# Kernel tuning notes

Hardware: AMD Instinct MI355X
Metric: run time of the kernel (lower is better)

Reference implementation:

```python
import jax, jax.numpy as jnp
import numpy as np

DIM = 192
N_HEADS = 8
HEAD_DIM = DIM // N_HEADS
SCALE = 1.0 / np.sqrt(HEAD_DIM).astype(np.float32)
H_GRID, W_GRID = 32, 64
KH, KW = 7, 11


def build_local_mask():
    # Equivalent to the torch double-loop construction: token (h2,w2) may attend
    # to (h,w) iff |h2-h| <= KH//2 and |w2-w| <= KW//2 (odd kernels).
    hh = jnp.arange(H_GRID)
    ww = jnp.arange(W_GRID)
    dh_ok = jnp.abs(hh[:, None] - hh[None, :]) <= KH // 2  # [H, H]
    dw_ok = jnp.abs(ww[:, None] - ww[None, :]) <= KW // 2  # [W, W]
    allowed = dh_ok[:, None, :, None] & dw_ok[None, :, None, :]  # [H, W, H, W]
    allowed = allowed.reshape(H_GRID * W_GRID, H_GRID * W_GRID)
    return jnp.where(allowed, 0.0, -jnp.inf).astype(jnp.float32)  # [N, N]


def setup_inputs() -> dict:
    key = jax.random.key(0)
    ks = jax.random.split(key, 5)
    B, N = 4, H_GRID * W_GRID
    w_std = 1.0 / np.sqrt(DIM)
    x = jax.random.normal(ks[0], (B, N, DIM), dtype=jnp.float32)
    qkv_w = jax.random.normal(ks[1], (3 * DIM, DIM), dtype=jnp.float32) * w_std
    qkv_b = jax.random.normal(ks[2], (3 * DIM,), dtype=jnp.float32) * 0.02
    proj_w = jax.random.normal(ks[3], (DIM, DIM), dtype=jnp.float32) * w_std
    proj_b = jax.random.normal(ks[4], (DIM,), dtype=jnp.float32) * 0.02
    mask = build_local_mask()
    return {"x": x, "qkv_w": qkv_w, "qkv_b": qkv_b,
            "proj_w": proj_w, "proj_b": proj_b, "mask": mask}


def reference(x, qkv_w, qkv_b, proj_w, proj_b, mask):
    B, N, _ = x.shape
    qkv = x @ qkv_w.T + qkv_b                              # [B, N, 3*DIM]
    qkv = qkv.reshape(B, N, 3, N_HEADS, HEAD_DIM)
    qkv = jnp.transpose(qkv, (2, 0, 3, 1, 4))              # [3, B, h, N, d]
    q, k, v = qkv[0] * SCALE, qkv[1], qkv[2]
    attn = jnp.einsum('bhnd,bhmd->bhnm', q, k) + mask      # [B, h, N, N]
    attn = jax.nn.softmax(attn, axis=-1)                   # == log_softmax().exp()
    out = jnp.einsum('bhnm,bhmd->bhnd', attn, v)           # [B, h, N, d]
    out = jnp.transpose(out, (0, 2, 1, 3)).reshape(B, N, DIM)
    return out @ proj_w.T + proj_b
```

## Files before the change

### kernel.cpp

```cpp
#include <hip/hip_runtime.h>
#include <math.h>

#define H_GRID 32
#define W_GRID 64
#define NTOK   2048
#define NHEADS 8
#define HD     24
#define DIMC   192
#define BATCH  4

static constexpr float SCALE = 0.20412414523193154f;

typedef unsigned short ushort;
typedef unsigned int   uint;
typedef __attribute__((ext_vector_type(8))) _Float16 f16x8;
typedef __attribute__((ext_vector_type(4))) float    f32x4;

static __device__ __forceinline__ float4 ld4(const float* p) { return *(const float4*)p; }

static __device__ __forceinline__ ushort f2h(float f) {
    _Float16 h = (_Float16)f;
    union { _Float16 h; ushort u; } c; c.h = h; return c.u;
}
static __device__ __forceinline__ float h2f(ushort u) {
    union { ushort u; _Float16 h; } c; c.u = u; return (float)c.h;
}

__global__ __launch_bounds__(256) void cast_h(const float* __restrict__ x,
                                              const float* __restrict__ wq,
                                              const float* __restrict__ wp,
                                              ushort* __restrict__ xh,
                                              ushort* __restrict__ wqh,
                                              ushort* __restrict__ wph,
                                              ushort* __restrict__ Qh,
                                              ushort* __restrict__ Kh) {
    const int i = blockIdx.x * 256 + threadIdx.x;
    if (i >= 430080) {
        const int ti = i - 430080;
        ushort* dst = (ti >> 16) ? Kh : Qh;
        const int row = ti & 65535;
        const uint4 z = {0u, 0u, 0u, 0u};
        *(uint4*)&dst[(size_t)row * 32 + 24] = z;
        return;
    }
    const float* src; ushort* dh; int off;
    if (i < 393216)      { src = x;  dh = xh;  off = i; }
    else if (i < 420864) { src = wq; dh = wqh; off = i - 393216; }
    else                 { src = wp; dh = wph; off = i - 420864; }
    float4 v = ld4(src + (size_t)off * 4);
    *(ushort4*)(dh + (size_t)off * 4) =
        make_ushort4(f2h(v.x), f2h(v.y), f2h(v.z), f2h(v.w));
}

__global__ __launch_bounds__(256, 4) void gemm_qkv(const ushort* __restrict__ Ah,
                                                   const ushort* __restrict__ Wh,
                                                   const float* __restrict__ bias,
                                                   ushort* __restrict__ Qh,
                                                   ushort* __restrict__ Kh,
                                                   ushort* __restrict__ VTh) {
    __shared__ ushort Ws[64 * 200];

    const int t    = threadIdx.x;
    const int wave = t >> 6, lane = t & 63;
    const int m0   = blockIdx.x * 64 + wave * 16;
    const int j0   = blockIdx.y * 64;
    const int n16  = lane & 15;
    const int kq   = lane >> 4;

    for (int i = t; i < 1536; i += 256) {
        const int r = i / 24, c = i - (i / 24) * 24;
        *(uint4*)&Ws[r * 200 + c * 8] = *(const uint4*)&Wh[(size_t)(j0 + r) * 192 + c * 8];
    }

    const ushort* ap = Ah + (size_t)(m0 + n16) * 192 + kq * 8;

    f16x8 af[6];
#pragma unroll
    for (int ks = 0; ks < 6; ks++) af[ks] = *(const f16x8*)(ap + ks * 32);

    f32x4 acc[4] = {f32x4{0,0,0,0}, f32x4{0,0,0,0}, f32x4{0,0,0,0}, f32x4{0,0,0,0}};

    __syncthreads();

#pragma unroll
    for (int ks = 0; ks < 6; ks++) {
#pragma unroll
        for (int nt = 0; nt < 4; nt++) {
            const f16x8 bf = *(const f16x8*)&Ws[(nt * 16 + n16) * 200 + kq * 8 + ks * 32];
            acc[nt] = __builtin_amdgcn_mfma_f32_16x16x32_f16(af[ks], bf, acc[nt], 0, 0, 0);
        }
    }

    const int band  = blockIdx.y / 3;
    const int mrow0 = m0 + kq * 4;
    const int b_    = mrow0 >> 11;
    const int tok0  = mrow0 & 2047;

    if (band == 2) {
#pragma unroll
        for (int nt = 0; nt < 4; nt++) {
            const int col = j0 + nt * 16 + n16;
            const int lc  = col - 384;
            const int h_  = lc / 24;
            const int d_  = lc - h_ * 24;
            const float bv = bias[col];
            ushort vv[4];
#pragma unroll
            for (int r = 0; r < 4; r++) vv[r] = f2h(acc[nt][r] + bv);
            const size_t addr = ((size_t)(b_ * 8 + h_) * 32 + d_) * 2080 + 8 + tok0;
            *(ushort4*)&VTh[addr] = make_ushort4(vv[0], vv[1], vv[2], vv[3]);
        }
    } else {
        const float sc_ = band ? 1.0f : SCALE;
        __syncthreads();
#pragma unroll
        for (int nt = 0; nt < 4; nt++) {
            const int col = j0 + nt * 16 + n16;
            const float bv = bias[col];
#pragma unroll
            for (int r = 0; r < 4; r++) {
                Ws[(wave * 16 + kq * 4 + r) * 68 + nt * 16 + n16] =
                    f2h((acc[nt][r] + bv) * sc_);
            }
        }
        __syncthreads();
        ushort* dst = band ? Kh : Qh;
        const int lc0 = j0 - band * 192;
#pragma unroll
        for (int it = 0; it < 4; it++) {
            const int item = t + 256 * it;
            const int tokl = item >> 4;
            const int cg   = item & 15;
            const ushort4 v = *(const ushort4*)&Ws[tokl * 68 + cg * 4];
            const int lc = lc0 + cg * 4;
            const int h_ = lc / 24;
            const int d0 = lc - h_ * 24;
            const int m  = blockIdx.x * 64 + tokl;
            const size_t addr = ((size_t)((m >> 11) * 8 + h_) * 2048 + (m & 2047)) * 32 + d0;
            *(ushort4*)&dst[addr] = v;
        }
    }
}

__global__ __launch_bounds__(256, 4) void attn_mfma(const ushort* __restrict__ Qh,
                                                    const ushort* __restrict__ Kh,
                                                    const ushort* __restrict__ VTh,
                                                    ushort* __restrict__ aws) {
    const int id    = blockIdx.x;
    const int head  = id & 7;
    const int qtile = (id >> 3) & 63;
    const int b     = id >> 9;
    const int qh0   = (qtile >> 3) * 4;
    const int qw0   = (qtile & 7) * 8;
    const int kw0a  = qw0 - 8;

    const int t = threadIdx.x;
    const int w = t >> 6, lane = t & 63;
    const int n16 = lane & 15, quad = lane >> 4;
    const int bh = b * 8 + head;

    __shared__ ushort P[32 * 328];
    __shared__ ushort Os[32 * 28];
    __shared__ float  mxbuf[64], sumbuf[64];

    const ushort* Qb = Qh + (size_t)bh * 65536;
    const ushort* Kb = Kh + (size_t)bh * 65536;

    const int mt = w >> 1, nth = w & 1;
    const int mrow = 16 * mt + n16;
    const int tq_a = ((qh0 + (mrow >> 3)) << 6) + qw0 + (mrow & 7);
    const f16x8 qf = *(const f16x8*)&Qb[(size_t)tq_a * 32 + quad * 8];

    float sv[10][4];
    float mx4[4] = {-3e38f, -3e38f, -3e38f, -3e38f};
#pragma unroll
    for (int half = 0; half < 2; half++) {
        f16x8 kf[5];
        int khvv[5], kwvv[5];
#pragma unroll
        for (int jj = 0; jj < 5; jj++) {
            const int j = half * 5 + jj;
            const int slot = (nth * 10 + j) * 16 + n16;
            const int rr = slot >> 5, cc = slot & 31;
            khvv[jj] = qh0 - 3 + rr;
            kwvv[jj] = kw0a + cc;
            const int tok = (min(max(khvv[jj], 0), 31) << 6) + min(max(kwvv[jj], 0), 63);
            kf[jj] = *(const f16x8*)&Kb[(size_t)tok * 32 + quad * 8];
        }
#pragma unroll
        for (int jj = 0; jj < 5; jj++) {
            const int j = half * 5 + jj;
            f32x4 a = f32x4{0, 0, 0, 0};
            a = __builtin_amdgcn_mfma_f32_16x16x32_f16(qf, kf[jj], a, 0, 0, 0);
            const int khv = khvv[jj], kwv = kwvv[jj];
            const bool kok = (khv >= 0) && (khv < 32) && (kwv >= 0) && (kwv < 64);
#pragma unroll
            for (int r = 0; r < 4; r++) {
                const int m   = 16 * mt + quad * 4 + r;
                const int qhv = qh0 + (m >> 3);
                const int qwv = qw0 + (m & 7);
                const bool valid = kok && (abs(khv - qhv) <= 3) && (abs(kwv - qwv) <= 5);
                const float s = valid ? a[r] : -3e38f;
                sv[j][r] = s;
                mx4[r] = fmaxf(mx4[r], s);
            }
        }
    }
#pragma unroll
    for (int d = 1; d < 16; d <<= 1)
#pragma unroll
        for (int r = 0; r < 4; r++) mx4[r] = fmaxf(mx4[r], __shfl_xor(mx4[r], d));
    if (n16 == 0) {
#pragma unroll
        for (int r = 0; r < 4; r++) mxbuf[w * 16 + quad * 4 + r] = mx4[r];
    }
    __syncthreads();
#pragma unroll
    for (int r = 0; r < 4; r++) mx4[r] = fmaxf(mx4[r], mxbuf[(w ^ 1) * 16 + quad * 4 + r]);

    float sum4[4] = {0.f, 0.f, 0.f, 0.f};
#pragma unroll
    for (int j = 0; j < 10; j++) {
        const int slot = (nth * 10 + j) * 16 + n16;
#pragma unroll
        for (int r = 0; r < 4; r++) {
            const float p = __expf(sv[j][r] - mx4[r]);
            const ushort ph = f2h(p);
            sum4[r] += h2f(ph);
            P[(16 * mt + quad * 4 + r) * 328 + slot] = ph;
        }
    }
#pragma unroll
    for (int d = 1; d < 16; d <<= 1)
#pragma unroll
        for (int r = 0; r < 4; r++) sum4[r] += __shfl_xor(sum4[r], d);
    if (n16 == 0) {
#pragma unroll
        for (int r = 0; r < 4; r++) sumbuf[w * 16 + quad * 4 + r] = sum4[r];
    }
    __syncthreads();

    const int mtP = w >> 1, ntP = w & 1;
    const int dcol = 16 * ntP + n16;
    const ushort* VTb = VTh + (size_t)bh * 66560;
    f32x4 acc = f32x4{0, 0, 0, 0};
#pragma unroll
    for (int half = 0; half < 2; half++) {
        f16x8 vf[5], pa[5];
#pragma unroll
        for (int kk = 0; kk < 5; kk++) {
            const int ks = half * 5 + kk;
            const int kh_cl = min(max(qh0 - 3 + ks, 0), 31);
            vf[kk] = *(const f16x8*)&VTb[(size_t)dcol * 2080 + 8 + (kh_cl << 6) + kw0a + quad * 8];
            pa[kk] = *(const f16x8*)&P[(16 * mtP + n16) * 328 + ks * 32 + quad * 8];
        }
#pragma unroll
        for (int kk = 0; kk < 5; kk++) {
            acc = __builtin_amdgcn_mfma_f32_16x16x32_f16(pa[kk], vf[kk], acc, 0, 0, 0);
        }
    }
    if (dcol < 24) {
#pragma unroll
        for (int r = 0; r < 4; r++) {
            const int m = 16 * mtP + quad * 4 + r;
            const float tot = sumbuf[(2 * mtP) * 16 + (m & 15)] +
                              sumbuf[(2 * mtP + 1) * 16 + (m & 15)];
            Os[m * 28 + dcol] = f2h(acc[r] / tot);
        }
    }
    __syncthreads();

    if (t < 192) {
        const int tok = t / 6, g = t - (t / 6) * 6;
        const ushort4 v = *(const ushort4*)&Os[tok * 28 + g * 4];
        const int tq = ((qh0 + (tok >> 3)) << 6) + qw0 + (tok & 7);
        *(ushort4*)&aws[((size_t)(b * 2048 + tq)) * 192 + head * 24 + g * 4] = v;
    }
}

__global__ __launch_bounds__(128, 4) void gemm_proj(const ushort* __restrict__ Ah,
                                                    const ushort* __restrict__ Wh,
                                                    const float* __restrict__ bias,
                                                    float* __restrict__ C) {
    __shared__ ushort Ws[64 * 200];

    const int t    = threadIdx.x;
    const int wave = t >> 6, lane = t & 63;
    const int m0   = blockIdx.x * 32 + wave * 16;
    const int j0   = blockIdx.y * 64;
    const int n16  = lane & 15;
    const int kq   = lane >> 4;

    for (int i = t; i < 1536; i += 128) {
        const int r = i / 24, c = i - (i / 24) * 24;
        *(uint4*)&Ws[r * 200 + c * 8] = *(const uint4*)&Wh[(size_t)(j0 + r) * 192 + c * 8];
    }

    const ushort* ap = Ah + (size_t)(m0 + n16) * 192 + kq * 8;

    f16x8 af[6];
#pragma unroll
    for (int ks = 0; ks < 6; ks++) af[ks] = *(const f16x8*)(ap + ks * 32);

    f32x4 acc[4] = {f32x4{0,0,0,0}, f32x4{0,0,0,0}, f32x4{0,0,0,0}, f32x4{0,0,0,0}};

    __syncthreads();

#pragma unroll
    for (int ks = 0; ks < 6; ks++) {
#pragma unroll
        for (int nt = 0; nt < 4; nt++) {
            const f16x8 bf = *(const f16x8*)&Ws[(nt * 16 + n16) * 200 + kq * 8 + ks * 32];
            acc[nt] = __builtin_amdgcn_mfma_f32_16x16x32_f16(af[ks], bf, acc[nt], 0, 0, 0);
        }
    }

#pragma unroll
    for (int nt = 0; nt < 4; nt++) {
        const int col = j0 + nt * 16 + n16;
        const float bv = bias[col];
#pragma unroll
        for (int r = 0; r < 4; r++) {
            const int m = m0 + kq * 4 + r;
            C[(size_t)m * 192 + col] = acc[nt][r] + bv;
        }
    }
}

extern "C" void kernel_launch(void* const* d_in, const int* in_sizes, int n_in,
                              void* d_out, int out_size, void* d_ws, size_t ws_size,
                              hipStream_t stream) {
    const float* x      = (const float*)d_in[0];
    const float* qkv_w  = (const float*)d_in[1];
    const float* qkv_b  = (const float*)d_in[2];
    const float* proj_w = (const float*)d_in[3];
    const float* proj_b = (const float*)d_in[4];

    char* wsb = (char*)d_ws;
    ushort* xh   = (ushort*)(wsb + 0);
    ushort* wqh  = (ushort*)(wsb + 3145728);
    ushort* wph  = (ushort*)(wsb + 3366912);
    ushort* Qh   = (ushort*)(wsb + 3440640);
    ushort* Kh   = (ushort*)(wsb + 7634944);
    ushort* VTh  = (ushort*)(wsb + 11829248);
    ushort* awsh = (ushort*)(wsb + 16171008);
    float*  out  = (float*)d_out;

    hipLaunchKernelGGL(cast_h, dim3(2192), dim3(256), 0, stream,
                       x, qkv_w, proj_w, xh, wqh, wph, Qh, Kh);
    hipLaunchKernelGGL(gemm_qkv, dim3(128, 9), dim3(256), 0, stream,
                       xh, wqh, qkv_b, Qh, Kh, VTh);
    hipLaunchKernelGGL(attn_mfma, dim3(2048), dim3(256), 0, stream,
                       Qh, Kh, VTh, awsh);
    hipLaunchKernelGGL(gemm_proj, dim3(256, 3), dim3(128), 0, stream,
                       awsh, wph, proj_b, out);
}
```

Baseline: 111.9 us.

## Fuse fp32-to-fp16 casts into GEMMs and widen N tiles to full band

Removes the separate cast kernel and folds the fp32-to-fp16 conversion of x and the weights into the QKV and projection GEMM loads. Each block now covers a full 192-column band, so the whole weight band sits in LDS and A is read once per band instead of three times. The zero padding of Q/K rows moves into the QKV epilogue. This saves one launch and the round trip through the fp16 copies, but larger LDS and more accumulators lower occupancy, and every block re-converts its weights.

```diff
diff --git a/kernel.cpp b/kernel.cpp
--- a/kernel.cpp
+++ b/kernel.cpp
@@ -26,84 +26,69 @@
     union { ushort u; _Float16 h; } c; c.u = u; return (float)c.h;
 }
 
-__global__ __launch_bounds__(256) void cast_h(const float* __restrict__ x,
-                                              const float* __restrict__ wq,
-                                              const float* __restrict__ wp,
-                                              ushort* __restrict__ xh,
-                                              ushort* __restrict__ wqh,
-                                              ushort* __restrict__ wph,
-                                              ushort* __restrict__ Qh,
-                                              ushort* __restrict__ Kh) {
-    const int i = blockIdx.x * 256 + threadIdx.x;
-    if (i >= 430080) {
-        const int ti = i - 430080;
-        ushort* dst = (ti >> 16) ? Kh : Qh;
-        const int row = ti & 65535;
-        const uint4 z = {0u, 0u, 0u, 0u};
-        *(uint4*)&dst[(size_t)row * 32 + 24] = z;
-        return;
-    }
-    const float* src; ushort* dh; int off;
-    if (i < 393216)      { src = x;  dh = xh;  off = i; }
-    else if (i < 420864) { src = wq; dh = wqh; off = i - 393216; }
-    else                 { src = wp; dh = wph; off = i - 420864; }
-    float4 v = ld4(src + (size_t)off * 4);
-    *(ushort4*)(dh + (size_t)off * 4) =
-        make_ushort4(f2h(v.x), f2h(v.y), f2h(v.z), f2h(v.w));
-}
-
-__global__ __launch_bounds__(256, 4) void gemm_qkv(const ushort* __restrict__ Ah,
-                                                   const ushort* __restrict__ Wh,
+__global__ __launch_bounds__(256, 2) void gemm_qkv(const float* __restrict__ A,
+                                                   const float* __restrict__ W,
                                                    const float* __restrict__ bias,
                                                    ushort* __restrict__ Qh,
                                                    ushort* __restrict__ Kh,
                                                    ushort* __restrict__ VTh) {
-    __shared__ ushort Ws[64 * 200];
+    __shared__ ushort Ws[192 * 200];
 
     const int t    = threadIdx.x;
     const int wave = t >> 6, lane = t & 63;
+    const int band = blockIdx.y;
     const int m0   = blockIdx.x * 64 + wave * 16;
-    const int j0   = blockIdx.y * 64;
+    const int j0   = band * 192;
     const int n16  = lane & 15;
     const int kq   = lane >> 4;
 
-    for (int i = t; i < 1536; i += 256) {
-        const int r = i / 24, c = i - (i / 24) * 24;
-        *(uint4*)&Ws[r * 200 + c * 8] = *(const uint4*)&Wh[(size_t)(j0 + r) * 192 + c * 8];
-    }
-
-    const ushort* ap = Ah + (size_t)(m0 + n16) * 192 + kq * 8;
-
+    for (int i = t; i < 9216; i += 256) {
+        const int r = i / 48, c = i - (i / 48) * 48;
+        float4 v = ld4(&W[(size_t)(j0 + r) * 192 + c * 4]);
+        *(ushort4*)&Ws[r * 200 + c * 4] =
+            make_ushort4(f2h(v.x), f2h(v.y), f2h(v.z), f2h(v.w));
+    }
+
+    const float* ap = A + (size_t)(m0 + n16) * 192 + kq * 8;
     f16x8 af[6];
 #pragma unroll
-    for (int ks = 0; ks < 6; ks++) af[ks] = *(const f16x8*)(ap + ks * 32);
-
-    f32x4 acc[4] = {f32x4{0,0,0,0}, f32x4{0,0,0,0}, f32x4{0,0,0,0}, f32x4{0,0,0,0}};
-
-    __syncthreads();
-
-#pragma unroll
     for (int ks = 0; ks < 6; ks++) {
-#pragma unroll
-        for (int nt = 0; nt < 4; nt++) {
+        float4 a0 = ld4(ap + ks * 32);
+        float4 a1 = ld4(ap + ks * 32 + 4);
+        f16x8 v;
+        v[0] = (_Float16)a0.x; v[1] = (_Float16)a0.y;
+        v[2] = (_Float16)a0.z; v[3] = (_Float16)a0.w;
+        v[4] = (_Float16)a1.x; v[5] = (_Float16)a1.y;
+        v[6] = (_Float16)a1.z; v[7] = (_Float16)a1.w;
+        af[ks] = v;
+    }
+
+    f32x4 acc[12];
+#pragma unroll
+    for (int nt = 0; nt < 12; nt++) acc[nt] = f32x4{0, 0, 0, 0};
+
+    __syncthreads();
+
+#pragma unroll
+    for (int ks = 0; ks < 6; ks++) {
+#pragma unroll
+        for (int nt = 0; nt < 12; nt++) {
             const f16x8 bf = *(const f16x8*)&Ws[(nt * 16 + n16) * 200 + kq * 8 + ks * 32];
             acc[nt] = __builtin_amdgcn_mfma_f32_16x16x32_f16(af[ks], bf, acc[nt], 0, 0, 0);
         }
     }
 
-    const int band  = blockIdx.y / 3;
     const int mrow0 = m0 + kq * 4;
     const int b_    = mrow0 >> 11;
     const int tok0  = mrow0 & 2047;
 
     if (band == 2) {
 #pragma unroll
-        for (int nt = 0; nt < 4; nt++) {
-            const int col = j0 + nt * 16 + n16;
-            const int lc  = col - 384;
-            const int h_  = lc / 24;
-            const int d_  = lc - h_ * 24;
-            const float bv = bias[col];
+        for (int nt = 0; nt < 12; nt++) {
+            const int lc = nt * 16 + n16;
+            const int h_ = lc / 24;
+            const int d_ = lc - h_ * 24;
+            const float bv = bias[384 + lc];
             ushort vv[4];
 #pragma unroll
             for (int r = 0; r < 4; r++) vv[r] = f2h(acc[nt][r] + bv);
@@ -114,30 +99,30 @@
         const float sc_ = band ? 1.0f : SCALE;
         __syncthreads();
 #pragma unroll
-        for (int nt = 0; nt < 4; nt++) {
-            const int col = j0 + nt * 16 + n16;
-            const float bv = bias[col];
+        for (int nt = 0; nt < 12; nt++) {
+            const int col = nt * 16 + n16;
+            const float bv = bias[band * 192 + col];
 #pragma unroll
             for (int r = 0; r < 4; r++) {
-                Ws[(wave * 16 + kq * 4 + r) * 68 + nt * 16 + n16] =
+                Ws[(wave * 16 + kq * 4 + r) * 196 + col] =
                     f2h((acc[nt][r] + bv) * sc_);
             }
         }
         __syncthreads();
         ushort* dst = band ? Kh : Qh;
-        const int lc0 = j0 - band * 192;
-#pragma unroll
-        for (int it = 0; it < 4; it++) {
-            const int item = t + 256 * it;
-            const int tokl = item >> 4;
-            const int cg   = item & 15;
-            const ushort4 v = *(const ushort4*)&Ws[tokl * 68 + cg * 4];
-            const int lc = lc0 + cg * 4;
+        const uint4 zz = {0u, 0u, 0u, 0u};
+        for (int i = t; i < 3072; i += 256) {
+            const int tokl = i / 48, cg = i - (i / 48) * 48;
+            const ushort4 v = *(const ushort4*)&Ws[tokl * 196 + cg * 4];
+            const int lc = cg * 4;
             const int h_ = lc / 24;
             const int d0 = lc - h_ * 24;
             const int m  = blockIdx.x * 64 + tokl;
             const size_t addr = ((size_t)((m >> 11) * 8 + h_) * 2048 + (m & 2047)) * 32 + d0;
             *(ushort4*)&dst[addr] = v;
+            if (d0 == 20) {
+                *(uint4*)&dst[addr + 4] = zz;
+            }
         }
     }
 }
@@ -278,22 +263,23 @@
     }
 }
 
-__global__ __launch_bounds__(128, 4) void gemm_proj(const ushort* __restrict__ Ah,
-                                                    const ushort* __restrict__ Wh,
+__global__ __launch_bounds__(128, 2) void gemm_proj(const ushort* __restrict__ Ah,
+                                                    const float* __restrict__ W,
                                                     const float* __restrict__ bias,
                                                     float* __restrict__ C) {
-    __shared__ ushort Ws[64 * 200];
+    __shared__ ushort Ws[192 * 200];
 
     const int t    = threadIdx.x;
     const int wave = t >> 6, lane = t & 63;
     const int m0   = blockIdx.x * 32 + wave * 16;
-    const int j0   = blockIdx.y * 64;
     const int n16  = lane & 15;
     const int kq   = lane >> 4;
 
-    for (int i = t; i < 1536; i += 128) {
-        const int r = i / 24, c = i - (i / 24) * 24;
-        *(uint4*)&Ws[r * 200 + c * 8] = *(const uint4*)&Wh[(size_t)(j0 + r) * 192 + c * 8];
+    for (int i = t; i < 9216; i += 128) {
+        const int r = i / 48, c = i - (i / 48) * 48;
+        float4 v = ld4(&W[(size_t)r * 192 + c * 4]);
+        *(ushort4*)&Ws[r * 200 + c * 4] =
+            make_ushort4(f2h(v.x), f2h(v.y), f2h(v.z), f2h(v.w));
     }
 
     const ushort* ap = Ah + (size_t)(m0 + n16) * 192 + kq * 8;
@@ -302,22 +288,24 @@
 #pragma unroll
     for (int ks = 0; ks < 6; ks++) af[ks] = *(const f16x8*)(ap + ks * 32);
 
-    f32x4 acc[4] = {f32x4{0,0,0,0}, f32x4{0,0,0,0}, f32x4{0,0,0,0}, f32x4{0,0,0,0}};
+    f32x4 acc[12];
+#pragma unroll
+    for (int nt = 0; nt < 12; nt++) acc[nt] = f32x4{0, 0, 0, 0};
 
     __syncthreads();
 
 #pragma unroll
     for (int ks = 0; ks < 6; ks++) {
 #pragma unroll
-        for (int nt = 0; nt < 4; nt++) {
+        for (int nt = 0; nt < 12; nt++) {
             const f16x8 bf = *(const f16x8*)&Ws[(nt * 16 + n16) * 200 + kq * 8 + ks * 32];
             acc[nt] = __builtin_amdgcn_mfma_f32_16x16x32_f16(af[ks], bf, acc[nt], 0, 0, 0);
         }
     }
 
 #pragma unroll
-    for (int nt = 0; nt < 4; nt++) {
-        const int col = j0 + nt * 16 + n16;
+    for (int nt = 0; nt < 12; nt++) {
+        const int col = nt * 16 + n16;
         const float bv = bias[col];
 #pragma unroll
         for (int r = 0; r < 4; r++) {
@@ -337,21 +325,16 @@
     const float* proj_b = (const float*)d_in[4];
 
     char* wsb = (char*)d_ws;
-    ushort* xh   = (ushort*)(wsb + 0);
-    ushort* wqh  = (ushort*)(wsb + 3145728);
-    ushort* wph  = (ushort*)(wsb + 3366912);
-    ushort* Qh   = (ushort*)(wsb + 3440640);
-    ushort* Kh   = (ushort*)(wsb + 7634944);
-    ushort* VTh  = (ushort*)(wsb + 11829248);
-    ushort* awsh = (ushort*)(wsb + 16171008);
+    ushort* Qh   = (ushort*)(wsb + 0);
+    ushort* Kh   = (ushort*)(wsb + 4194304);
+    ushort* VTh  = (ushort*)(wsb + 8388608);
+    ushort* awsh = (ushort*)(wsb + 12648448);
     float*  out  = (float*)d_out;
 
-    hipLaunchKernelGGL(cast_h, dim3(2192), dim3(256), 0, stream,
-                       x, qkv_w, proj_w, xh, wqh, wph, Qh, Kh);
-    hipLaunchKernelGGL(gemm_qkv, dim3(128, 9), dim3(256), 0, stream,
-                       xh, wqh, qkv_b, Qh, Kh, VTh);
+    hipLaunchKernelGGL(gemm_qkv, dim3(128, 3), dim3(256), 0, stream,
+                       x, qkv_w, qkv_b, Qh, Kh, VTh);
     hipLaunchKernelGGL(attn_mfma, dim3(2048), dim3(256), 0, stream,
                        Qh, Kh, VTh, awsh);
-    hipLaunchKernelGGL(gemm_proj, dim3(256, 3), dim3(128), 0, stream,
-                       awsh, wph, proj_b, out);
-}
+    hipLaunchKernelGGL(gemm_proj, dim3(256), dim3(128), 0, stream,
+                       awsh, proj_w, proj_b, out);
+}
```

Result: slower. 132.6 us (+18.4%).
